# Performance work log

Measured on AMD Instinct MI355X. Metric: run time of the kernel, lower is better.

The kernel has to match this reference:

```python
import jax, jax.numpy as jnp
import numpy as np

NEG_INF = -1e38


def _wkv_scan(time_decay, time_first, key, value):
    # key, value: [B, S, D]; time_decay/time_first: [D]
    B, S, D = key.shape
    w = -jnp.exp(time_decay)  # decay applied additively in log-space

    def step(carry, kv):
        num, den, mx = carry
        k, v = kv  # [B, D]
        # output with current token boosted by time_first
        m_out = jnp.maximum(mx, k + time_first)
        e1 = jnp.exp(mx - m_out)
        e2 = jnp.exp(k + time_first - m_out)
        out = (e1 * num + e2 * v) / (e1 * den + e2)
        # state update with decay
        m_new = jnp.maximum(mx + w, k)
        e1 = jnp.exp(mx + w - m_new)
        e2 = jnp.exp(k - m_new)
        return (e1 * num + e2 * v, e1 * den + e2, m_new), out

    init = (jnp.zeros((B, D), jnp.float32),
            jnp.zeros((B, D), jnp.float32),
            jnp.full((B, D), NEG_INF, jnp.float32))
    kv = (jnp.moveaxis(key, 1, 0), jnp.moveaxis(value, 1, 0))  # [S, B, D]
    _, out = jax.lax.scan(step, init, kv)
    return jnp.moveaxis(out, 0, 1)  # [B, S, D]


def setup_inputs() -> dict:
    key = jax.random.key(0)
    ks = jax.random.split(key, 10)
    B, S, H = 4, 2048, 2048
    D = H  # attention_hidden_size
    return {
        "hidden": jax.random.normal(ks[0], (B, S, H), jnp.float32),
        "time_decay": jax.random.normal(ks[1], (D,), jnp.float32),
        "time_first": jax.random.normal(ks[2], (D,), jnp.float32),
        "time_mix_key": jax.random.uniform(ks[3], (1, 1, H), jnp.float32),
        "time_mix_value": jax.random.uniform(ks[4], (1, 1, H), jnp.float32),
        "time_mix_receptance": jax.random.uniform(ks[5], (1, 1, H), jnp.float32),
        "Wk": jax.random.normal(ks[6], (D, H), jnp.float32) / np.sqrt(H),  # torch Linear weight [out, in]
        "Wv": jax.random.normal(ks[7], (D, H), jnp.float32) / np.sqrt(H),
        "Wr": jax.random.normal(ks[8], (D, H), jnp.float32) / np.sqrt(H),
        "Wo": jax.random.normal(ks[9], (H, D), jnp.float32) / np.sqrt(D),
    }


def reference(hidden, time_decay, time_first, time_mix_key, time_mix_value,
              time_mix_receptance, Wk, Wv, Wr, Wo):
    # time_shift: prepend a zero timestep, drop the last (ZeroPad2d((0,0,1,-1)))
    shifted = jnp.pad(hidden, ((0, 0), (1, 0), (0, 0)))[:, :-1]
    xk = hidden * time_mix_key + shifted * (1.0 - time_mix_key)
    xv = hidden * time_mix_value + shifted * (1.0 - time_mix_value)
    xr = hidden * time_mix_receptance + shifted * (1.0 - time_mix_receptance)
    k = jnp.einsum('bsh,dh->bsd', xk, Wk)
    v = jnp.einsum('bsh,dh->bsd', xv, Wv)
    r = jax.nn.sigmoid(jnp.einsum('bsh,dh->bsd', xr, Wr))
    rwkv = _wkv_scan(time_decay, time_first, k, v)
    return jnp.einsum('bsd,hd->bsh', r * rwkv, Wo)
```

## Files before the change

### kernel.cpp

```cpp
#include <hip/hip_runtime.h>


typedef __attribute__((ext_vector_type(8))) short s16x8;
typedef __attribute__((ext_vector_type(16))) float f32x16;

__device__ __forceinline__ unsigned short f2bf(float f) {
  union { float f; unsigned u; } v; v.f = f;
  unsigned r = v.u + 0x7fffu + ((v.u >> 16) & 1u);
  return (unsigned short)(r >> 16);
}
__device__ __forceinline__ float bf2f(unsigned short h) {
  union { unsigned u; float f; } v; v.u = ((unsigned)h) << 16; return v.f;
}
__device__ __forceinline__ void gload_lds16(const void* g, void* l) {
  __builtin_amdgcn_global_load_lds(
      (const __attribute__((address_space(1))) void*)g,
      (__attribute__((address_space(3))) void*)l, 16, 0, 0);
}


__global__ void conv_bf16(const float4* __restrict__ src, ushort4* __restrict__ dst, int n4) {
  int i = blockIdx.x * blockDim.x + threadIdx.x;
  if (i >= n4) return;
  float4 v = src[i];
  ushort4 o;
  o.x = f2bf(v.x); o.y = f2bf(v.y); o.z = f2bf(v.z); o.w = f2bf(v.w);
  dst[i] = o;
}


__global__ void prep_mix3(const float4* __restrict__ hidden,
                          const float4* __restrict__ tmk,
                          const float4* __restrict__ tmv,
                          const float4* __restrict__ tmr,
                          ushort4* __restrict__ xk, ushort4* __restrict__ xv,
                          ushort4* __restrict__ xr,
                          int S, int H4, long long total4) {
  long long i = (long long)blockIdx.x * blockDim.x + threadIdx.x;
  if (i >= total4) return;
  int h4 = (int)(i % H4);
  long long sb = i / H4;
  int s = (int)(sb % S);
  float4 cur = hidden[i];
  float4 prev = make_float4(0.f, 0.f, 0.f, 0.f);
  if (s > 0) prev = hidden[i - H4];
  float4 mk = tmk[h4], mv = tmv[h4], mr = tmr[h4];
  ushort4 ok, ov, orr;
  ok.x = f2bf(cur.x * mk.x + prev.x * (1.f - mk.x));
  ok.y = f2bf(cur.y * mk.y + prev.y * (1.f - mk.y));
  ok.z = f2bf(cur.z * mk.z + prev.z * (1.f - mk.z));
  ok.w = f2bf(cur.w * mk.w + prev.w * (1.f - mk.w));
  ov.x = f2bf(cur.x * mv.x + prev.x * (1.f - mv.x));
  ov.y = f2bf(cur.y * mv.y + prev.y * (1.f - mv.y));
  ov.z = f2bf(cur.z * mv.z + prev.z * (1.f - mv.z));
  ov.w = f2bf(cur.w * mv.w + prev.w * (1.f - mv.w));
  orr.x = f2bf(cur.x * mr.x + prev.x * (1.f - mr.x));
  orr.y = f2bf(cur.y * mr.y + prev.y * (1.f - mr.y));
  orr.z = f2bf(cur.z * mr.z + prev.z * (1.f - mr.z));
  orr.w = f2bf(cur.w * mr.w + prev.w * (1.f - mr.w));
  xk[i] = ok; xv[i] = ov; xr[i] = orr;
}


template <int EPI>
__global__ __launch_bounds__(512) void gemm_bt(
    const unsigned short* __restrict__ A, const unsigned short* __restrict__ B,
    float* __restrict__ Cf, unsigned short* __restrict__ Cb,
    int M, int N, int K) {
  __shared__ unsigned short lds[4][16384];

  const int tid = threadIdx.x;
  const int wave = tid >> 6;
  const int lane = tid & 63;

  const int nwg = (int)gridDim.x;
  const int q = nwg >> 3;
  const int wg = (blockIdx.x & 7) * q + (blockIdx.x >> 3);
  const int GM = M >> 8;
  const int bm = (wg % GM) * 256;
  const int bn = (wg / GM) * 256;

  const int wm = (wave >> 2) * 128;
  const int wn = (wave & 3) * 64;
  const int lrow = lane & 31;
  const int lq = lane >> 5;

  f32x16 acc[4][2] = {};

  const int srow = tid >> 2;
  const int sg = ((tid & 3) ^ ((srow >> 1) & 3)) * 8;
  const unsigned short* gA0 = A + (long long)(bm + srow) * K + sg;
  const unsigned short* gA1 = A + (long long)(bm + 128 + srow) * K + sg;
  const unsigned short* gB0 = B + (long long)(bn + srow) * K + sg;
  const unsigned short* gB1 = B + (long long)(bn + 128 + srow) * K + sg;

#define STAGE_A(sl)                                            \
  {                                                            \
    unsigned short* dst = &lds[sl][0] + wave * 512;            \
    gload_lds16(gA0, dst);                                     \
    gload_lds16(gA1, dst + 4096);                              \
    gA0 += 32; gA1 += 32;                                      \
  }
#define STAGE_B(sl)                                            \
  {                                                            \
    unsigned short* dst = &lds[sl][0] + wave * 512;            \
    gload_lds16(gB0, dst + 8192);                              \
    gload_lds16(gB1, dst + 12288);                             \
    gB0 += 32; gB1 += 32;                                      \
  }

  int offA[4][2], offB[2][2];
#pragma unroll
  for (int mt = 0; mt < 4; ++mt)
#pragma unroll
    for (int h = 0; h < 2; ++h) {
      int R = wm + mt * 32 + lrow;
      int c = h * 2 + lq;
      offA[mt][h] = R * 32 + ((c ^ ((R >> 1) & 3)) * 8);
    }
#pragma unroll
  for (int nt = 0; nt < 2; ++nt)
#pragma unroll
    for (int h = 0; h < 2; ++h) {
      int Cc = wn + nt * 32 + lrow;
      int c = h * 2 + lq;
      offB[nt][h] = 8192 + Cc * 32 + ((c ^ ((Cc >> 1) & 3)) * 8);
    }

  const int NT = K >> 5;

  STAGE_A(0); STAGE_B(0);
  STAGE_A(1); STAGE_B(1);
  STAGE_A(2); STAGE_B(2);
  asm volatile("s_waitcnt vmcnt(8)" ::: "memory");
  __builtin_amdgcn_sched_barrier(0);
  __builtin_amdgcn_s_barrier();

  for (int t = 0; t < NT; ++t) {
    const unsigned short* sb = &lds[t & 3][0];
    const bool pf = (t + 3 < NT);
    s16x8 af[2][2], bfr[2][2];

#pragma unroll
    for (int mt = 0; mt < 2; ++mt)
#pragma unroll
      for (int h = 0; h < 2; ++h)
        af[mt][h] = *(const s16x8*)(sb + offA[mt][h]);
#pragma unroll
    for (int nt = 0; nt < 2; ++nt)
#pragma unroll
      for (int h = 0; h < 2; ++h)
        bfr[nt][h] = *(const s16x8*)(sb + offB[nt][h]);

    if (pf) STAGE_A((t + 3) & 3);
    __builtin_amdgcn_s_barrier();

    __builtin_amdgcn_s_setprio(1);
#pragma unroll
    for (int h = 0; h < 2; ++h)
#pragma unroll
      for (int mt = 0; mt < 2; ++mt)
#pragma unroll
        for (int nt = 0; nt < 2; ++nt)
          acc[mt][nt] = __builtin_amdgcn_mfma_f32_32x32x16_bf16(
              af[mt][h], bfr[nt][h], acc[mt][nt], 0, 0, 0);
    __builtin_amdgcn_s_setprio(0);
    __builtin_amdgcn_s_barrier();

    s16x8 ag[2][2];
#pragma unroll
    for (int mt = 0; mt < 2; ++mt)
#pragma unroll
      for (int h = 0; h < 2; ++h)
        ag[mt][h] = *(const s16x8*)(sb + offA[2 + mt][h]);

    if (pf) STAGE_B((t + 3) & 3);

    if (pf) {
      asm volatile("s_waitcnt vmcnt(8)" ::: "memory");
    } else if (t + 3 == NT) {
      asm volatile("s_waitcnt vmcnt(4)" ::: "memory");
    } else if (t + 2 == NT) {
      asm volatile("s_waitcnt vmcnt(0)" ::: "memory");
    }
    __builtin_amdgcn_sched_barrier(0);
    __builtin_amdgcn_s_barrier();

    __builtin_amdgcn_s_setprio(1);
#pragma unroll
    for (int h = 0; h < 2; ++h)
#pragma unroll
      for (int mt = 0; mt < 2; ++mt)
#pragma unroll
        for (int nt = 0; nt < 2; ++nt)
          acc[2 + mt][nt] = __builtin_amdgcn_mfma_f32_32x32x16_bf16(
              ag[mt][h], bfr[nt][h], acc[2 + mt][nt], 0, 0, 0);
    __builtin_amdgcn_s_setprio(0);
    __builtin_amdgcn_s_barrier();
  }
#undef STAGE_A
#undef STAGE_B

#pragma unroll
  for (int mt = 0; mt < 4; ++mt)
#pragma unroll
    for (int nt = 0; nt < 2; ++nt)
#pragma unroll
      for (int r = 0; r < 16; ++r) {
        int row = bm + wm + mt * 32 + (r & 3) + 8 * (r >> 2) + 4 * lq;
        int col = bn + wn + nt * 32 + lrow;
        float v = acc[mt][nt][r];
        long long idx = (long long)row * N + col;
        if (EPI == 0) {
          Cf[idx] = v;
        } else if (EPI == 1) {
          float s = 1.f / (1.f + __expf(-v));
          Cb[idx] = f2bf(s);
        } else {
          Cb[idx] = f2bf(v);
        }
      }
}


#define NEG_INF_F (-1e38f)

__global__ void scan_phase1(const unsigned short* __restrict__ kb,
                            const unsigned short* __restrict__ vb,
                            const float* __restrict__ td,
                            float* __restrict__ locN, float* __restrict__ locD,
                            float* __restrict__ locM,
                            int S, int D, int C, int L) {
  int t = blockIdx.x * blockDim.x + threadIdx.x;
  int d = t % D;
  int c = (t / D) % C;
  int b = t / (D * C);
  float w = -__expf(td[d]);
  float num = 0.f, den = 0.f, m = NEG_INF_F;
  long long base = ((long long)(b * S + c * L)) * D + d;
  for (int i = 0; i < L; ++i) {
    float kk = bf2f(kb[base]);
    float vv = bf2f(vb[base]);
    base += D;
    float mn = fmaxf(m + w, kk);
    float e1 = __expf(m + w - mn);
    float e2 = __expf(kk - mn);
    num = e1 * num + e2 * vv;
    den = e1 * den + e2;
    m = mn;
  }
  int o = (b * C + c) * D + d;
  locN[o] = num; locD[o] = den; locM[o] = m;
}

__global__ void scan_phase2(const float* __restrict__ td,
                            const float* __restrict__ locN, const float* __restrict__ locD,
                            const float* __restrict__ locM,
                            float* __restrict__ inN, float* __restrict__ inD,
                            float* __restrict__ inM,
                            int Bc, int D, int C, int L) {
  int t = blockIdx.x * blockDim.x + threadIdx.x;
  if (t >= Bc * D) return;
  int d = t % D, b = t / D;
  float w = -__expf(td[d]);
  float Lw = (float)L * w;
  float num = 0.f, den = 0.f, m = NEG_INF_F;
  for (int c = 0; c < C; ++c) {
    int o = (b * C + c) * D + d;
    inN[o] = num; inD[o] = den; inM[o] = m;
    float sm = m + Lw;
    float lm = locM[o];
    float m2 = fmaxf(sm, lm);
    float e1 = __expf(sm - m2);
    float e2 = __expf(lm - m2);
    num = e1 * num + e2 * locN[o];
    den = e1 * den + e2 * locD[o];
    m = m2;
  }
}

__global__ void scan_phase3(const unsigned short* __restrict__ kb,
                            const unsigned short* __restrict__ vb,
                            const unsigned short* __restrict__ rb,
                            const float* __restrict__ td, const float* __restrict__ tfirst,
                            const float* __restrict__ inN, const float* __restrict__ inD,
                            const float* __restrict__ inM,
                            unsigned short* __restrict__ rr,
                            int S, int D, int C, int L) {
  int t = blockIdx.x * blockDim.x + threadIdx.x;
  int d = t % D;
  int c = (t / D) % C;
  int b = t / (D * C);
  float w = -__expf(td[d]);
  float tfd = tfirst[d];
  int o = (b * C + c) * D + d;
  float num = inN[o], den = inD[o], m = inM[o];
  long long base = ((long long)(b * S + c * L)) * D + d;
  for (int i = 0; i < L; ++i) {
    float kk = bf2f(kb[base]);
    float vv = bf2f(vb[base]);
    float rv = bf2f(rb[base]);
    float ktf = kk + tfd;
    float mo = fmaxf(m, ktf);
    float e1 = __expf(m - mo);
    float e2 = __expf(ktf - mo);
    float out = (e1 * num + e2 * vv) / (e1 * den + e2);
    rr[base] = f2bf(out * rv);
    float mn = fmaxf(m + w, kk);
    e1 = __expf(m + w - mn);
    e2 = __expf(kk - mn);
    num = e1 * num + e2 * vv;
    den = e1 * den + e2;
    m = mn;
    base += D;
  }
}


extern "C" void kernel_launch(void* const* d_in, const int* in_sizes, int n_in,
                              void* d_out, int out_size, void* d_ws, size_t ws_size,
                              hipStream_t stream) {
  const float* hidden = (const float*)d_in[0];
  const float* td  = (const float*)d_in[1];
  const float* tfi = (const float*)d_in[2];
  const float* tmk = (const float*)d_in[3];
  const float* tmv = (const float*)d_in[4];
  const float* tmr = (const float*)d_in[5];
  const float* Wk  = (const float*)d_in[6];
  const float* Wv  = (const float*)d_in[7];
  const float* Wr  = (const float*)d_in[8];
  const float* Wo  = (const float*)d_in[9];
  float* out = (float*)d_out;

  const int H = in_sizes[1];
  const int D = H;
  const long long BS = (long long)in_sizes[0] / H;
  const int S = 2048;
  const int B = (int)(BS / S);
  const int C = 32, L = S / C;

  char* ws = (char*)d_ws;
  const size_t MB = 1u << 20;
  unsigned short* W_b = (unsigned short*)(ws + 0 * MB);
  unsigned short* X   = (unsigned short*)(ws + 8 * MB);
  unsigned short* Y   = (unsigned short*)(ws + 40 * MB);
  unsigned short* Z   = (unsigned short*)(ws + 72 * MB);
  float* locN         = (float*)(ws + 104 * MB);
  float* locD         = (float*)(ws + 105 * MB);
  float* locM         = (float*)(ws + 106 * MB);
  float* inN          = (float*)(ws + 107 * MB);
  float* inD          = (float*)(ws + 108 * MB);
  float* inM          = (float*)(ws + 109 * MB);
  unsigned short* kb  = (unsigned short*)out;

  int n4w = H * H / 4;
  int cbk = (n4w + 255) / 256;
  long long total4 = BS * H / 4;
  int pbk = (int)((total4 + 255) / 256);
  int nwg = (int)((BS / 256) * (D / 256));

  prep_mix3<<<pbk, 256, 0, stream>>>((const float4*)hidden,
                                     (const float4*)tmk, (const float4*)tmv, (const float4*)tmr,
                                     (ushort4*)X, (ushort4*)Y, (ushort4*)Z, S, H / 4, total4);

  conv_bf16<<<cbk, 256, 0, stream>>>((const float4*)Wk, (ushort4*)W_b, n4w);
  gemm_bt<2><<<nwg, 512, 0, stream>>>(X, W_b, nullptr, kb, (int)BS, D, H);

  conv_bf16<<<cbk, 256, 0, stream>>>((const float4*)Wv, (ushort4*)W_b, n4w);
  gemm_bt<2><<<nwg, 512, 0, stream>>>(Y, W_b, nullptr, X, (int)BS, D, H);

  conv_bf16<<<cbk, 256, 0, stream>>>((const float4*)Wr, (ushort4*)W_b, n4w);
  gemm_bt<1><<<nwg, 512, 0, stream>>>(Z, W_b, nullptr, Y, (int)BS, D, H);

  int nscan = B * C * D;
  scan_phase1<<<nscan / 256, 256, 0, stream>>>(kb, X, td, locN, locD, locM, S, D, C, L);
  scan_phase2<<<(B * D + 255) / 256, 256, 0, stream>>>(td, locN, locD, locM, inN, inD, inM, B, D, C, L);
  scan_phase3<<<nscan / 256, 256, 0, stream>>>(kb, X, Y, td, tfi, inN, inD, inM, Z, S, D, C, L);

  conv_bf16<<<cbk, 256, 0, stream>>>((const float4*)Wo, (ushort4*)W_b, n4w);
  gemm_bt<0><<<nwg, 512, 0, stream>>>(Z, W_b, out, nullptr, (int)BS, H, D);
}
```

Measured before the change: 554.9 us.

## Software-pipeline LDS fragment reads across K iterations and halve barriers

```diff
diff --git a/kernel.cpp b/kernel.cpp
--- a/kernel.cpp
+++ b/kernel.cpp
@@ -63,7 +63,7 @@
 
 
 template <int EPI>
-__global__ __launch_bounds__(512) void gemm_bt(
+__global__ __launch_bounds__(512, 2) void gemm_bt(
     const unsigned short* __restrict__ A, const unsigned short* __restrict__ B,
     float* __restrict__ Cf, unsigned short* __restrict__ Cb,
     int M, int N, int K) {
@@ -129,75 +129,84 @@
 
   const int NT = K >> 5;
 
+  s16x8 a0[2][2][2];
+  s16x8 a1[2][2];
+  s16x8 bfr[2][2];
+
   STAGE_A(0); STAGE_B(0);
   STAGE_A(1); STAGE_B(1);
   STAGE_A(2); STAGE_B(2);
   asm volatile("s_waitcnt vmcnt(8)" ::: "memory");
   __builtin_amdgcn_sched_barrier(0);
   __builtin_amdgcn_s_barrier();
-
-  for (int t = 0; t < NT; ++t) {
-    const unsigned short* sb = &lds[t & 3][0];
-    const bool pf = (t + 3 < NT);
-    s16x8 af[2][2], bfr[2][2];
-
-#pragma unroll
-    for (int mt = 0; mt < 2; ++mt)
-#pragma unroll
-      for (int h = 0; h < 2; ++h)
-        af[mt][h] = *(const s16x8*)(sb + offA[mt][h]);
-#pragma unroll
-    for (int nt = 0; nt < 2; ++nt)
-#pragma unroll
-      for (int h = 0; h < 2; ++h)
-        bfr[nt][h] = *(const s16x8*)(sb + offB[nt][h]);
-
-    if (pf) STAGE_A((t + 3) & 3);
-    __builtin_amdgcn_s_barrier();
-
-    __builtin_amdgcn_s_setprio(1);
+  __builtin_amdgcn_sched_barrier(0);
+#pragma unroll
+  for (int mt = 0; mt < 2; ++mt)
 #pragma unroll
     for (int h = 0; h < 2; ++h)
-#pragma unroll
-      for (int mt = 0; mt < 2; ++mt)
-#pragma unroll
-        for (int nt = 0; nt < 2; ++nt)
-          acc[mt][nt] = __builtin_amdgcn_mfma_f32_32x32x16_bf16(
-              af[mt][h], bfr[nt][h], acc[mt][nt], 0, 0, 0);
-    __builtin_amdgcn_s_setprio(0);
-    __builtin_amdgcn_s_barrier();
-
-    s16x8 ag[2][2];
-#pragma unroll
-    for (int mt = 0; mt < 2; ++mt)
-#pragma unroll
-      for (int h = 0; h < 2; ++h)
-        ag[mt][h] = *(const s16x8*)(sb + offA[2 + mt][h]);
-
-    if (pf) STAGE_B((t + 3) & 3);
-
-    if (pf) {
-      asm volatile("s_waitcnt vmcnt(8)" ::: "memory");
-    } else if (t + 3 == NT) {
-      asm volatile("s_waitcnt vmcnt(4)" ::: "memory");
-    } else if (t + 2 == NT) {
-      asm volatile("s_waitcnt vmcnt(0)" ::: "memory");
-    }
-    __builtin_amdgcn_sched_barrier(0);
-    __builtin_amdgcn_s_barrier();
-
-    __builtin_amdgcn_s_setprio(1);
+      a0[0][mt][h] = *(const s16x8*)(&lds[0][0] + offA[mt][h]);
+#pragma unroll
+  for (int nt = 0; nt < 2; ++nt)
 #pragma unroll
     for (int h = 0; h < 2; ++h)
-#pragma unroll
-      for (int mt = 0; mt < 2; ++mt)
-#pragma unroll
-        for (int nt = 0; nt < 2; ++nt)
-          acc[2 + mt][nt] = __builtin_amdgcn_mfma_f32_32x32x16_bf16(
-              ag[mt][h], bfr[nt][h], acc[2 + mt][nt], 0, 0, 0);
-    __builtin_amdgcn_s_setprio(0);
-    __builtin_amdgcn_s_barrier();
-  }
+      bfr[nt][h] = *(const s16x8*)(&lds[0][0] + offB[nt][h]);
+
+#define K_ITER(T, P, Q)                                                       \
+  {                                                                           \
+    const int t_ = (T);                                                       \
+    const unsigned short* sb = &lds[t_ & 3][0];                               \
+    const unsigned short* sbn = &lds[(t_ + 1) & 3][0];                        \
+    const bool pf = (t_ + 3 < NT);                                            \
+    const bool rd = (t_ + 1 < NT);                                            \
+                                                       \
+    if (pf) STAGE_A((t_ + 3) & 3);                                            \
+    _Pragma("unroll") for (int mt = 0; mt < 2; ++mt)                          \
+      _Pragma("unroll") for (int h = 0; h < 2; ++h)                           \
+        a1[mt][h] = *(const s16x8*)(sb + offA[2 + mt][h]);                    \
+    __builtin_amdgcn_s_setprio(1);                                            \
+    _Pragma("unroll") for (int h = 0; h < 2; ++h)                             \
+      _Pragma("unroll") for (int mt = 0; mt < 2; ++mt)                        \
+        _Pragma("unroll") for (int nt = 0; nt < 2; ++nt)                      \
+          acc[mt][nt] = __builtin_amdgcn_mfma_f32_32x32x16_bf16(              \
+              a0[P][mt][h], bfr[nt][h], acc[mt][nt], 0, 0, 0);                \
+    __builtin_amdgcn_s_setprio(0);                                            \
+                                                       \
+    if (pf) STAGE_B((t_ + 3) & 3);                                            \
+    if (pf) {                                                                 \
+      asm volatile("s_waitcnt vmcnt(8)" ::: "memory");                        \
+    } else if (t_ + 3 == NT) {                                                \
+      asm volatile("s_waitcnt vmcnt(4)" ::: "memory");                        \
+    } else if (t_ + 2 == NT) {                                                \
+      asm volatile("s_waitcnt vmcnt(0)" ::: "memory");                        \
+    }                                                                         \
+    __builtin_amdgcn_sched_barrier(0);                                        \
+    __builtin_amdgcn_s_barrier();                                             \
+    __builtin_amdgcn_sched_barrier(0);                                        \
+    if (rd) {                                                                 \
+      _Pragma("unroll") for (int mt = 0; mt < 2; ++mt)                        \
+        _Pragma("unroll") for (int h = 0; h < 2; ++h)                         \
+          a0[Q][mt][h] = *(const s16x8*)(sbn + offA[mt][h]);                  \
+    }                                                                         \
+    __builtin_amdgcn_s_setprio(1);                                            \
+    _Pragma("unroll") for (int h = 0; h < 2; ++h)                             \
+      _Pragma("unroll") for (int mt = 0; mt < 2; ++mt)                        \
+        _Pragma("unroll") for (int nt = 0; nt < 2; ++nt)                      \
+          acc[2 + mt][nt] = __builtin_amdgcn_mfma_f32_32x32x16_bf16(          \
+              a1[mt][h], bfr[nt][h], acc[2 + mt][nt], 0, 0, 0);               \
+    __builtin_amdgcn_s_setprio(0);                                            \
+    if (rd) {                                                                 \
+      _Pragma("unroll") for (int nt = 0; nt < 2; ++nt)                        \
+        _Pragma("unroll") for (int h = 0; h < 2; ++h)                         \
+          bfr[nt][h] = *(const s16x8*)(sbn + offB[nt][h]);                    \
+    }                                                                         \
+    __builtin_amdgcn_s_barrier();                                             \
+  }
+
+  for (int t = 0; t < NT; t += 2) {
+    K_ITER(t, 0, 1);
+    K_ITER(t + 1, 1, 0);
+  }
+#undef K_ITER
 #undef STAGE_A
 #undef STAGE_B
 
```

New measurement: 551.3 us. No clear change (-0.6%).

## Restructure GEMM main loop to BK=64 with split A/B LDS ring buffers

Applied to the files above, without the earlier changes.

```diff
diff --git a/kernel.cpp b/kernel.cpp
--- a/kernel.cpp
+++ b/kernel.cpp
@@ -63,11 +63,12 @@
 
 
 template <int EPI>
-__global__ __launch_bounds__(512) void gemm_bt(
+__global__ __launch_bounds__(512, 2) void gemm_bt(
     const unsigned short* __restrict__ A, const unsigned short* __restrict__ B,
     float* __restrict__ Cf, unsigned short* __restrict__ Cb,
     int M, int N, int K) {
-  __shared__ unsigned short lds[4][16384];
+  __shared__ unsigned short ldsA[3 * 16384];
+  __shared__ unsigned short ldsB[2 * 16384];
 
   const int tid = threadIdx.x;
   const int wave = tid >> 6;
@@ -87,116 +88,124 @@
 
   f32x16 acc[4][2] = {};
 
-  const int srow = tid >> 2;
-  const int sg = ((tid & 3) ^ ((srow >> 1) & 3)) * 8;
-  const unsigned short* gA0 = A + (long long)(bm + srow) * K + sg;
-  const unsigned short* gA1 = A + (long long)(bm + 128 + srow) * K + sg;
-  const unsigned short* gB0 = B + (long long)(bn + srow) * K + sg;
-  const unsigned short* gB1 = B + (long long)(bn + 128 + srow) * K + sg;
-
-#define STAGE_A(sl)                                            \
-  {                                                            \
-    unsigned short* dst = &lds[sl][0] + wave * 512;            \
-    gload_lds16(gA0, dst);                                     \
-    gload_lds16(gA1, dst + 4096);                              \
-    gA0 += 32; gA1 += 32;                                      \
-  }
-#define STAGE_B(sl)                                            \
-  {                                                            \
-    unsigned short* dst = &lds[sl][0] + wave * 512;            \
-    gload_lds16(gB0, dst + 8192);                              \
-    gload_lds16(gB1, dst + 12288);                             \
-    gB0 += 32; gB1 += 32;                                      \
-  }
-
-  int offA[4][2], offB[2][2];
-#pragma unroll
-  for (int mt = 0; mt < 4; ++mt)
-#pragma unroll
-    for (int h = 0; h < 2; ++h) {
-      int R = wm + mt * 32 + lrow;
-      int c = h * 2 + lq;
-      offA[mt][h] = R * 32 + ((c ^ ((R >> 1) & 3)) * 8);
-    }
-#pragma unroll
-  for (int nt = 0; nt < 2; ++nt)
-#pragma unroll
-    for (int h = 0; h < 2; ++h) {
-      int Cc = wn + nt * 32 + lrow;
-      int c = h * 2 + lq;
-      offB[nt][h] = 8192 + Cc * 32 + ((c ^ ((Cc >> 1) & 3)) * 8);
-    }
-
-  const int NT = K >> 5;
-
-  STAGE_A(0); STAGE_B(0);
-  STAGE_A(1); STAGE_B(1);
-  STAGE_A(2); STAGE_B(2);
-  asm volatile("s_waitcnt vmcnt(8)" ::: "memory");
+  const int srow = tid >> 3;
+  const int scol = ((tid & 7) ^ (srow & 7)) * 8;
+  const unsigned short* gA = A + (long long)(bm + srow) * K + scol;
+  const unsigned short* gB = B + (long long)(bn + srow) * K + scol;
+  const int rstep = K << 6;
+
+#define STAGE_A(slot)                                                \
+  {                                                                  \
+    unsigned short* d = ldsA + (slot) * 16384 + wave * 512;          \
+    gload_lds16(gA, d);                                              \
+    gload_lds16(gA + rstep, d + 4096);                               \
+    gload_lds16(gA + 2 * rstep, d + 8192);                           \
+    gload_lds16(gA + 3 * rstep, d + 12288);                          \
+    gA += 64;                                                        \
+  }
+#define STAGE_B(slot)                                                \
+  {                                                                  \
+    unsigned short* d = ldsB + (slot) * 16384 + wave * 512;          \
+    gload_lds16(gB, d);                                              \
+    gload_lds16(gB + rstep, d + 4096);                               \
+    gload_lds16(gB + 2 * rstep, d + 8192);                           \
+    gload_lds16(gB + 3 * rstep, d + 12288);                          \
+    gB += 64;                                                        \
+  }
+
+  int sA[4], sB[4];
+#pragma unroll
+  for (int ks = 0; ks < 4; ++ks) {
+    int c = (((2 * ks + lq) ^ (lane & 7)) * 8);
+    sA[ks] = (wm + lrow) * 64 + c;
+    sB[ks] = (wn + lrow) * 64 + c;
+  }
+
+  const int NT = K >> 6;
+
+  s16x8 a01[2][4], a23[2][4], bfr[2][4];
+
+  int aS0 = 0, aS1 = 1, aS2 = 2, bS = 0;
+
+  STAGE_A(0);
+  STAGE_B(0);
+  STAGE_A(1);
+  asm volatile("s_waitcnt vmcnt(4)" ::: "memory");
   __builtin_amdgcn_sched_barrier(0);
   __builtin_amdgcn_s_barrier();
+  __builtin_amdgcn_sched_barrier(0);
+#pragma unroll
+  for (int mt = 0; mt < 2; ++mt)
+#pragma unroll
+    for (int ks = 0; ks < 4; ++ks)
+      a01[mt][ks] = *(const s16x8*)(ldsA + sA[ks] + mt * 2048);
+#pragma unroll
+  for (int nt = 0; nt < 2; ++nt)
+#pragma unroll
+    for (int ks = 0; ks < 4; ++ks)
+      bfr[nt][ks] = *(const s16x8*)(ldsB + sB[ks] + nt * 2048);
 
   for (int t = 0; t < NT; ++t) {
-    const unsigned short* sb = &lds[t & 3][0];
-    const bool pf = (t + 3 < NT);
-    s16x8 af[2][2], bfr[2][2];
-
-#pragma unroll
-    for (int mt = 0; mt < 2; ++mt)
-#pragma unroll
-      for (int h = 0; h < 2; ++h)
-        af[mt][h] = *(const s16x8*)(sb + offA[mt][h]);
-#pragma unroll
-    for (int nt = 0; nt < 2; ++nt)
-#pragma unroll
-      for (int h = 0; h < 2; ++h)
-        bfr[nt][h] = *(const s16x8*)(sb + offB[nt][h]);
-
-    if (pf) STAGE_A((t + 3) & 3);
-    __builtin_amdgcn_s_barrier();
-
+    if (t + 2 < NT) STAGE_A(aS2);
+    if (t + 1 < NT) STAGE_B(bS ^ 1);
+    {
+      const unsigned short* sa = ldsA + aS0 * 16384;
+#pragma unroll
+      for (int mt = 0; mt < 2; ++mt)
+#pragma unroll
+        for (int ks = 0; ks < 4; ++ks)
+          a23[mt][ks] = *(const s16x8*)(sa + sA[ks] + (2 + mt) * 2048);
+    }
     __builtin_amdgcn_s_setprio(1);
 #pragma unroll
-    for (int h = 0; h < 2; ++h)
+    for (int ks = 0; ks < 4; ++ks)
 #pragma unroll
       for (int mt = 0; mt < 2; ++mt)
 #pragma unroll
         for (int nt = 0; nt < 2; ++nt)
           acc[mt][nt] = __builtin_amdgcn_mfma_f32_32x32x16_bf16(
-              af[mt][h], bfr[nt][h], acc[mt][nt], 0, 0, 0);
+              a01[mt][ks], bfr[nt][ks], acc[mt][nt], 0, 0, 0);
     __builtin_amdgcn_s_setprio(0);
-    __builtin_amdgcn_s_barrier();
-
-    s16x8 ag[2][2];
-#pragma unroll
-    for (int mt = 0; mt < 2; ++mt)
-#pragma unroll
-      for (int h = 0; h < 2; ++h)
-        ag[mt][h] = *(const s16x8*)(sb + offA[2 + mt][h]);
-
-    if (pf) STAGE_B((t + 3) & 3);
-
-    if (pf) {
-      asm volatile("s_waitcnt vmcnt(8)" ::: "memory");
-    } else if (t + 3 == NT) {
+
+    if (t + 2 < NT) {
       asm volatile("s_waitcnt vmcnt(4)" ::: "memory");
-    } else if (t + 2 == NT) {
+    } else if (t + 1 < NT) {
       asm volatile("s_waitcnt vmcnt(0)" ::: "memory");
     }
     __builtin_amdgcn_sched_barrier(0);
     __builtin_amdgcn_s_barrier();
-
+    __builtin_amdgcn_sched_barrier(0);
+
+    if (t + 1 < NT) {
+      const unsigned short* sa = ldsA + aS1 * 16384;
+#pragma unroll
+      for (int mt = 0; mt < 2; ++mt)
+#pragma unroll
+        for (int ks = 0; ks < 4; ++ks)
+          a01[mt][ks] = *(const s16x8*)(sa + sA[ks] + mt * 2048);
+    }
     __builtin_amdgcn_s_setprio(1);
 #pragma unroll
-    for (int h = 0; h < 2; ++h)
+    for (int ks = 0; ks < 4; ++ks)
 #pragma unroll
       for (int mt = 0; mt < 2; ++mt)
 #pragma unroll
         for (int nt = 0; nt < 2; ++nt)
           acc[2 + mt][nt] = __builtin_amdgcn_mfma_f32_32x32x16_bf16(
-              ag[mt][h], bfr[nt][h], acc[2 + mt][nt], 0, 0, 0);
+              a23[mt][ks], bfr[nt][ks], acc[2 + mt][nt], 0, 0, 0);
     __builtin_amdgcn_s_setprio(0);
+    if (t + 1 < NT) {
+      const unsigned short* sbp = ldsB + (bS ^ 1) * 16384;
+#pragma unroll
+      for (int nt = 0; nt < 2; ++nt)
+#pragma unroll
+        for (int ks = 0; ks < 4; ++ks)
+          bfr[nt][ks] = *(const s16x8*)(sbp + sB[ks] + nt * 2048);
+    }
     __builtin_amdgcn_s_barrier();
+
+    int tmp = aS0; aS0 = aS1; aS1 = aS2; aS2 = tmp;
+    bS ^= 1;
   }
 #undef STAGE_A
 #undef STAGE_B
```

New measurement: 577.3 us. 4.0% more time.

## Switch GEMM to 16x16x32 MFMA tiles with explicit LDS wait scheduling

Applied to the files above, without the earlier changes.

```diff
diff --git a/kernel.cpp b/kernel.cpp
--- a/kernel.cpp
+++ b/kernel.cpp
@@ -2,7 +2,7 @@
 
 
 typedef __attribute__((ext_vector_type(8))) short s16x8;
-typedef __attribute__((ext_vector_type(16))) float f32x16;
+typedef __attribute__((ext_vector_type(4))) float f32x4;
 
 __device__ __forceinline__ unsigned short f2bf(float f) {
   union { float f; unsigned u; } v; v.f = f;
@@ -63,11 +63,11 @@
 
 
 template <int EPI>
-__global__ __launch_bounds__(512) void gemm_bt(
+__global__ __launch_bounds__(512, 2) void gemm_bt(
     const unsigned short* __restrict__ A, const unsigned short* __restrict__ B,
     float* __restrict__ Cf, unsigned short* __restrict__ Cb,
     int M, int N, int K) {
-  __shared__ unsigned short lds[4][16384];
+  __shared__ unsigned short lds[4 * 16384];
 
   const int tid = threadIdx.x;
   const int wave = tid >> 6;
@@ -82,10 +82,10 @@
 
   const int wm = (wave >> 2) * 128;
   const int wn = (wave & 3) * 64;
-  const int lrow = lane & 31;
-  const int lq = lane >> 5;
-
-  f32x16 acc[4][2] = {};
+  const int l15 = lane & 15;
+  const int lg = lane >> 4;
+
+  f32x4 acc[8][4] = {};
 
   const int srow = tid >> 2;
   const int sg = ((tid & 3) ^ ((srow >> 1) & 3)) * 8;
@@ -96,36 +96,30 @@
 
 #define STAGE_A(sl)                                            \
   {                                                            \
-    unsigned short* dst = &lds[sl][0] + wave * 512;            \
+    unsigned short* dst = lds + (sl) * 16384 + wave * 512;     \
     gload_lds16(gA0, dst);                                     \
     gload_lds16(gA1, dst + 4096);                              \
     gA0 += 32; gA1 += 32;                                      \
   }
 #define STAGE_B(sl)                                            \
   {                                                            \
-    unsigned short* dst = &lds[sl][0] + wave * 512;            \
+    unsigned short* dst = lds + (sl) * 16384 + wave * 512;     \
     gload_lds16(gB0, dst + 8192);                              \
     gload_lds16(gB1, dst + 12288);                             \
     gB0 += 32; gB1 += 32;                                      \
   }
 
-  int offA[4][2], offB[2][2];
-#pragma unroll
-  for (int mt = 0; mt < 4; ++mt)
-#pragma unroll
-    for (int h = 0; h < 2; ++h) {
-      int R = wm + mt * 32 + lrow;
-      int c = h * 2 + lq;
-      offA[mt][h] = R * 32 + ((c ^ ((R >> 1) & 3)) * 8);
-    }
-#pragma unroll
-  for (int nt = 0; nt < 2; ++nt)
-#pragma unroll
-    for (int h = 0; h < 2; ++h) {
-      int Cc = wn + nt * 32 + lrow;
-      int c = h * 2 + lq;
-      offB[nt][h] = 8192 + Cc * 32 + ((c ^ ((Cc >> 1) & 3)) * 8);
-    }
+  int offA[8], offB[4];
+#pragma unroll
+  for (int mi = 0; mi < 8; ++mi) {
+    int R = wm + mi * 16 + l15;
+    offA[mi] = R * 32 + ((lg ^ ((R >> 1) & 3)) * 8);
+  }
+#pragma unroll
+  for (int ni = 0; ni < 4; ++ni) {
+    int R = wn + ni * 16 + l15;
+    offB[ni] = 8192 + R * 32 + ((lg ^ ((R >> 1) & 3)) * 8);
+  }
 
   const int NT = K >> 5;
 
@@ -137,45 +131,34 @@
   __builtin_amdgcn_s_barrier();
 
   for (int t = 0; t < NT; ++t) {
-    const unsigned short* sb = &lds[t & 3][0];
+    const unsigned short* sb = lds + (t & 3) * 16384;
     const bool pf = (t + 3 < NT);
-    s16x8 af[2][2], bfr[2][2];
-
-#pragma unroll
-    for (int mt = 0; mt < 2; ++mt)
-#pragma unroll
-      for (int h = 0; h < 2; ++h)
-        af[mt][h] = *(const s16x8*)(sb + offA[mt][h]);
-#pragma unroll
-    for (int nt = 0; nt < 2; ++nt)
-#pragma unroll
-      for (int h = 0; h < 2; ++h)
-        bfr[nt][h] = *(const s16x8*)(sb + offB[nt][h]);
-
+
+    s16x8 a[4], b[4];
+#pragma unroll
+    for (int mi = 0; mi < 4; ++mi) a[mi] = *(const s16x8*)(sb + offA[mi]);
+#pragma unroll
+    for (int ni = 0; ni < 4; ++ni) b[ni] = *(const s16x8*)(sb + offB[ni]);
     if (pf) STAGE_A((t + 3) & 3);
+    __builtin_amdgcn_sched_barrier(0);
     __builtin_amdgcn_s_barrier();
-
+    asm volatile("s_waitcnt lgkmcnt(0)" ::: "memory");
+    __builtin_amdgcn_sched_barrier(0);
     __builtin_amdgcn_s_setprio(1);
 #pragma unroll
-    for (int h = 0; h < 2; ++h)
-#pragma unroll
-      for (int mt = 0; mt < 2; ++mt)
-#pragma unroll
-        for (int nt = 0; nt < 2; ++nt)
-          acc[mt][nt] = __builtin_amdgcn_mfma_f32_32x32x16_bf16(
-              af[mt][h], bfr[nt][h], acc[mt][nt], 0, 0, 0);
+    for (int mi = 0; mi < 4; ++mi)
+#pragma unroll
+      for (int ni = 0; ni < 4; ++ni)
+        acc[mi][ni] = __builtin_amdgcn_mfma_f32_16x16x32_bf16(
+            a[mi], b[ni], acc[mi][ni], 0, 0, 0);
     __builtin_amdgcn_s_setprio(0);
+    __builtin_amdgcn_sched_barrier(0);
     __builtin_amdgcn_s_barrier();
 
-    s16x8 ag[2][2];
-#pragma unroll
-    for (int mt = 0; mt < 2; ++mt)
-#pragma unroll
-      for (int h = 0; h < 2; ++h)
-        ag[mt][h] = *(const s16x8*)(sb + offA[2 + mt][h]);
-
+    s16x8 a2[4];
+#pragma unroll
+    for (int mi = 0; mi < 4; ++mi) a2[mi] = *(const s16x8*)(sb + offA[4 + mi]);
     if (pf) STAGE_B((t + 3) & 3);
-
     if (pf) {
       asm volatile("s_waitcnt vmcnt(8)" ::: "memory");
     } else if (t + 3 == NT) {
@@ -185,31 +168,31 @@
     }
     __builtin_amdgcn_sched_barrier(0);
     __builtin_amdgcn_s_barrier();
-
+    asm volatile("s_waitcnt lgkmcnt(0)" ::: "memory");
+    __builtin_amdgcn_sched_barrier(0);
     __builtin_amdgcn_s_setprio(1);
 #pragma unroll
-    for (int h = 0; h < 2; ++h)
-#pragma unroll
-      for (int mt = 0; mt < 2; ++mt)
-#pragma unroll
-        for (int nt = 0; nt < 2; ++nt)
-          acc[2 + mt][nt] = __builtin_amdgcn_mfma_f32_32x32x16_bf16(
-              ag[mt][h], bfr[nt][h], acc[2 + mt][nt], 0, 0, 0);
+    for (int mi = 0; mi < 4; ++mi)
+#pragma unroll
+      for (int ni = 0; ni < 4; ++ni)
+        acc[4 + mi][ni] = __builtin_amdgcn_mfma_f32_16x16x32_bf16(
+            a2[mi], b[ni], acc[4 + mi][ni], 0, 0, 0);
     __builtin_amdgcn_s_setprio(0);
+    __builtin_amdgcn_sched_barrier(0);
     __builtin_amdgcn_s_barrier();
   }
 #undef STAGE_A
 #undef STAGE_B
 
 #pragma unroll
-  for (int mt = 0; mt < 4; ++mt)
-#pragma unroll
-    for (int nt = 0; nt < 2; ++nt)
-#pragma unroll
-      for (int r = 0; r < 16; ++r) {
-        int row = bm + wm + mt * 32 + (r & 3) + 8 * (r >> 2) + 4 * lq;
-        int col = bn + wn + nt * 32 + lrow;
-        float v = acc[mt][nt][r];
+  for (int mi = 0; mi < 8; ++mi)
+#pragma unroll
+    for (int ni = 0; ni < 4; ++ni)
+#pragma unroll
+      for (int r = 0; r < 4; ++r) {
+        int row = bm + wm + mi * 16 + lg * 4 + r;
+        int col = bn + wn + ni * 16 + l15;
+        float v = acc[mi][ni][r];
         long long idx = (long long)row * N + col;
         if (EPI == 0) {
           Cf[idx] = v;
```

Measured after the change: 544.2 us. Within noise of the previous version (-1.9%).
